# Kernel tuning notes

Measured on AMD Instinct MI355X. Metric: run time of the kernel, lower is better.

The kernel has to match this reference:

```python
import jax, jax.numpy as jnp
import numpy as np

SPATIAL_SHAPES = np.array([[100, 150], [50, 75], [25, 38], [13, 19]], dtype=np.int64)


def setup_inputs() -> dict:
    key = jax.random.key(0)
    k1, k2, k3 = jax.random.split(key, 3)
    B, heads, d = 1, 8, 32
    L, P = SPATIAL_SHAPES.shape[0], 4
    n_tokens = int(SPATIAL_SHAPES.prod(axis=1).sum())  # 19947
    Q = n_tokens
    value = jax.random.normal(k1, (B, n_tokens, heads, d), dtype=jnp.float32)
    sampling_locations = jax.random.uniform(k2, (B, Q, heads, L, P, 2), dtype=jnp.float32)
    aw = jax.random.uniform(k3, (B, Q, heads, L, P), dtype=jnp.float32)
    # normalize like the real module (softmax over L*P); keeps magnitudes realistic
    attention_weights = aw / aw.sum(axis=(-2, -1), keepdims=True)
    level_start = np.concatenate([[0], np.cumsum(SPATIAL_SHAPES.prod(axis=1))[:-1]]).astype(np.int64)
    return {
        'value': value,
        'value_spatial_shapes': jnp.asarray(SPATIAL_SHAPES),
        'value_level_start_index': jnp.asarray(level_start),
        'sampling_locations': sampling_locations,
        'attention_weights': attention_weights,
        'im2col_step': 64,
    }


def _sample_level(v, loc, Hh, Ww):
    """Bilinear grid_sample (align_corners=False, zero padding).
    v:   [B, heads, Hh*Ww, D]
    loc: [B, Q, heads, P, 2] normalized in [0,1]
    returns [B, heads, Q, P, D]
    """
    B, Q, heads, P, _ = loc.shape
    D = v.shape[-1]
    # grid = 2*loc - 1; pixel coord = (grid+1)*size/2 - 0.5  ==  loc*size - 0.5
    x = loc[..., 0] * Ww - 0.5
    y = loc[..., 1] * Hh - 0.5
    x0f = jnp.floor(x)
    y0f = jnp.floor(y)
    wx1 = x - x0f
    wy1 = y - y0f
    x0 = x0f.astype(jnp.int32)
    y0 = y0f.astype(jnp.int32)

    def gather(xi, yi):
        valid = ((xi >= 0) & (xi < Ww) & (yi >= 0) & (yi < Hh)).astype(v.dtype)
        idx = jnp.clip(yi, 0, Hh - 1) * Ww + jnp.clip(xi, 0, Ww - 1)  # [B,Q,heads,P]
        idx_t = idx.transpose(0, 2, 1, 3).reshape(B, heads, Q * P, 1)
        g = jnp.take_along_axis(v, idx_t, axis=2)  # [B,heads,Q*P,D]
        g = g.reshape(B, heads, Q, P, D)
        return g, valid.transpose(0, 2, 1, 3)[..., None]

    g00, m00 = gather(x0, y0)
    g01, m01 = gather(x0 + 1, y0)
    g10, m10 = gather(x0, y0 + 1)
    g11, m11 = gather(x0 + 1, y0 + 1)
    wx1t = wx1.transpose(0, 2, 1, 3)[..., None]
    wy1t = wy1.transpose(0, 2, 1, 3)[..., None]
    wx0t = 1.0 - wx1t
    wy0t = 1.0 - wy1t
    return (g00 * m00 * (wx0t * wy0t) + g01 * m01 * (wx1t * wy0t)
            + g10 * m10 * (wx0t * wy1t) + g11 * m11 * (wx1t * wy1t))


def msda_forward(value, spatial_shapes_np, sampling_locations, attention_weights):
    B, n_tokens, heads, D = value.shape
    Q = sampling_locations.shape[1]
    areas = [int(h) * int(w) for h, w in spatial_shapes_np]
    # value per level as [B, heads, H*W, D]
    v_bhnd = value.transpose(0, 2, 1, 3)  # [B, heads, N, D]
    out = jnp.zeros((B, Q, heads, D), dtype=value.dtype)
    start = 0
    for lvl, (Hh, Ww) in enumerate(spatial_shapes_np):
        Hh, Ww = int(Hh), int(Ww)
        v_l = jax.lax.slice_in_dim(v_bhnd, start, start + Hh * Ww, axis=2)
        loc_l = sampling_locations[:, :, :, lvl]  # [B,Q,heads,P,2]
        sampled = _sample_level(v_l, loc_l, Hh, Ww)  # [B,heads,Q,P,D]
        aw_l = attention_weights[:, :, :, lvl]  # [B,Q,heads,P]
        out = out + jnp.einsum('bhqpd,bqhp->bqhd', sampled, aw_l)
        start += Hh * Ww
    return out.reshape(B, Q, heads * D)


def reference(value, value_spatial_shapes, value_level_start_index, sampling_locations, attention_weights, im2col_step):
    spatial_shapes_np = np.asarray(jax.device_get(value_spatial_shapes))
    return msda_forward(value, spatial_shapes_np, sampling_locations, attention_weights)
```

## Files before the change

### kernel.cpp

```cpp
#include <hip/hip_runtime.h>


typedef float    f32x4 __attribute__((ext_vector_type(4)));
typedef float    f32x8 __attribute__((ext_vector_type(8)));
typedef _Float16 f16x8 __attribute__((ext_vector_type(8)));

constexpr int HEADS = 8;
constexpr int DCH   = 32;
constexpr int NSP   = 16;
constexpr int NQ    = 19947;
constexpr int QPB   = 64;
constexpr int HSTR  = NQ * DCH;
constexpr int NVAL  = NQ * HEADS * DCH;

__global__ __launch_bounds__(256)
void cvt_kernel(const float* __restrict__ value, _Float16* __restrict__ ws)
{
    const int i = blockIdx.x * 256 + threadIdx.x;
    if (i >= NQ * HEADS * 4) return;
    const int c8 = i & 3;
    const int h  = (i >> 2) & 7;
    const int t  = i >> 5;
    const float* src = value + (size_t)t * 256 + h * 32 + c8 * 8;
    const f32x4 a = __builtin_nontemporal_load((const f32x4*)src);
    const f32x4 b = __builtin_nontemporal_load((const f32x4*)(src + 4));
    const f32x8 v = {a.x, a.y, a.z, a.w, b.x, b.y, b.z, b.w};
    const f16x8 o = __builtin_convertvector(v, f16x8);
    *(f16x8*)(ws + (size_t)h * HSTR + t * 32 + c8 * 8) = o;
}

template <bool F16>
__global__ __launch_bounds__(256)
void msda_fwd_kernel(const void* __restrict__ valuev,
                     const float* __restrict__ loc,
                     const float* __restrict__ attw,
                     float* __restrict__ out)
{
    __shared__ float s_loc[QPB][33];
    __shared__ float s_aw [QPB][17];

    const int h    = blockIdx.x & 7;
    const int qblk = blockIdx.x >> 3;
    const int q0   = qblk * QPB;
    const int t    = threadIdx.x;

#pragma unroll
    for (int it = 0; it < 2; ++it) {
        const int idx = t + it * 256;
        const int sub = idx >> 3, j = idx & 7;
        const int q = q0 + sub;
        if (q < NQ) {
            const f32x4 v = __builtin_nontemporal_load(
                (const f32x4*)(loc + ((size_t)(q * HEADS + h)) * (NSP * 2) + j * 4));
            const int l = j >> 1;
            const float fW = (l == 0) ? 150.f : (l == 1) ? 75.f : (l == 2) ? 38.f : 19.f;
            const float fH = (l == 0) ? 100.f : (l == 1) ? 50.f : (l == 2) ? 25.f : 13.f;
            s_loc[sub][j * 4 + 0] = v.x * fW - 0.5f;
            s_loc[sub][j * 4 + 1] = v.y * fH - 0.5f;
            s_loc[sub][j * 4 + 2] = v.z * fW - 0.5f;
            s_loc[sub][j * 4 + 3] = v.w * fH - 0.5f;
        }
    }
    {
        const int sub = t >> 2, j = t & 3;
        const int q = q0 + sub;
        if (q < NQ) {
            const f32x4 w = __builtin_nontemporal_load(
                (const f32x4*)(attw + ((size_t)(q * HEADS + h)) * NSP + j * 4));
            s_aw[sub][j * 4 + 0] = w.x;
            s_aw[sub][j * 4 + 1] = w.y;
            s_aw[sub][j * 4 + 2] = w.z;
            s_aw[sub][j * 4 + 3] = w.w;
        }
    }
    __syncthreads();

    const int sub = t >> 2;
    const int j   = t & 2 * 2;
    const int jj  = t & 3;
    const int q   = q0 + sub;
    if (q >= NQ) return;
    (void)j;

    const _Float16* vf16 = (const _Float16*)valuev + (size_t)h * HSTR + jj * 8;
    const float*    vf32 = (const float*)valuev + h * DCH + jj * 8;

    f32x8 accA = {0.f, 0.f, 0.f, 0.f, 0.f, 0.f, 0.f, 0.f};
    f32x8 accB = {0.f, 0.f, 0.f, 0.f, 0.f, 0.f, 0.f, 0.f};

#pragma unroll
    for (int l = 0; l < 4; ++l) {
        const int W = (l == 0) ? 150 : (l == 1) ? 75 : (l == 2) ? 38 : 19;
        const int H = (l == 0) ? 100 : (l == 1) ? 50 : (l == 2) ? 25 : 13;
        const int S = (l == 0) ? 0 : (l == 1) ? 15000 : (l == 2) ? 18750 : 19700;
#pragma unroll
        for (int p = 0; p < 4; ++p) {
            const int sp = l * 4 + p;
            const float x  = s_loc[sub][sp * 2 + 0];
            const float y  = s_loc[sub][sp * 2 + 1];
            const float aw = s_aw[sub][sp];

            const float x0f = floorf(x);
            const float y0f = floorf(y);
            const float wx1 = x - x0f;
            const float wy1 = y - y0f;
            const float wx0 = 1.f - wx1;
            const float wy0 = 1.f - wy1;

            const int x0 = (int)x0f, y0 = (int)y0f;
            const int x1 = x0 + 1,   y1 = y0 + 1;

            const float awy0 = aw * wy0;
            const float awy1 = aw * wy1;
            const float wx0m = ((unsigned)x0 < (unsigned)W) ? wx0  : 0.f;
            const float wx1m = ((unsigned)x1 < (unsigned)W) ? wx1  : 0.f;
            const float wy0m = ((unsigned)y0 < (unsigned)H) ? awy0 : 0.f;
            const float wy1m = ((unsigned)y1 < (unsigned)H) ? awy1 : 0.f;
            const float c00 = wy0m * wx0m;
            const float c01 = wy0m * wx1m;
            const float c10 = wy1m * wx0m;
            const float c11 = wy1m * wx1m;

            const int cx0 = max(x0, 0), cx1 = min(x1, W - 1);
            const int cy0 = max(y0, 0), cy1 = min(y1, H - 1);
            const int r0 = S + cy0 * W;
            const int r1 = S + cy1 * W;
            const int i00 = r0 + cx0;
            const int i01 = r0 + cx1;
            const int i10 = r1 + cx0;
            const int i11 = r1 + cx1;

            f32x8* accp = (l < 2) ? &accA : &accB;

            if constexpr (F16) {
                const f16x8 g00 = *(const f16x8*)(vf16 + (size_t)i00 * 32);
                const f16x8 g01 = *(const f16x8*)(vf16 + (size_t)i01 * 32);
                const f16x8 g10 = *(const f16x8*)(vf16 + (size_t)i10 * 32);
                const f16x8 g11 = *(const f16x8*)(vf16 + (size_t)i11 * 32);
#pragma unroll
                for (int k = 0; k < 8; ++k) {
                    (*accp)[k] += c00 * (float)g00[k];
                    (*accp)[k] += c01 * (float)g01[k];
                    (*accp)[k] += c10 * (float)g10[k];
                    (*accp)[k] += c11 * (float)g11[k];
                }
            } else {
                const f32x4 a0 = *(const f32x4*)(vf32 + ((size_t)i00 << 8));
                const f32x4 a1 = *(const f32x4*)(vf32 + ((size_t)i00 << 8) + 4);
                const f32x4 b0 = *(const f32x4*)(vf32 + ((size_t)i01 << 8));
                const f32x4 b1 = *(const f32x4*)(vf32 + ((size_t)i01 << 8) + 4);
                const f32x4 c0 = *(const f32x4*)(vf32 + ((size_t)i10 << 8));
                const f32x4 c1 = *(const f32x4*)(vf32 + ((size_t)i10 << 8) + 4);
                const f32x4 d0_ = *(const f32x4*)(vf32 + ((size_t)i11 << 8));
                const f32x4 d1 = *(const f32x4*)(vf32 + ((size_t)i11 << 8) + 4);
#pragma unroll
                for (int k = 0; k < 4; ++k) {
                    (*accp)[k]     += c00 * a0[k] + c01 * b0[k] + c10 * c0[k] + c11 * d0_[k];
                    (*accp)[k + 4] += c00 * a1[k] + c01 * b1[k] + c10 * c1[k] + c11 * d1[k];
                }
            }
        }
    }

    const f32x8 acc = accA + accB;
    float* op = out + (size_t)(q * HEADS + h) * DCH + jj * 8;
    const f32x4 lo = {acc[0], acc[1], acc[2], acc[3]};
    const f32x4 hi = {acc[4], acc[5], acc[6], acc[7]};
    __builtin_nontemporal_store(lo, (f32x4*)op);
    __builtin_nontemporal_store(hi, (f32x4*)(op + 4));
}

extern "C" void kernel_launch(void* const* d_in, const int* in_sizes, int n_in,
                              void* d_out, int out_size, void* d_ws, size_t ws_size,
                              hipStream_t stream) {
    const float* value = (const float*)d_in[0];
    const float* loc   = (const float*)d_in[3];
    const float* attw  = (const float*)d_in[4];
    float* out = (float*)d_out;

    const int qblocks = (NQ + QPB - 1) / QPB;
    const int grid = qblocks * HEADS;

    const size_t f16_bytes = (size_t)NVAL * sizeof(_Float16);
    if (ws_size >= f16_bytes) {
        _Float16* ws = (_Float16*)d_ws;
        const int cgrid = (NQ * HEADS * 4 + 255) / 256;
        cvt_kernel<<<cgrid, 256, 0, stream>>>(value, ws);
        msda_fwd_kernel<true><<<grid, 256, 0, stream>>>(ws, loc, attw, out);
    } else {
        msda_fwd_kernel<false><<<grid, 256, 0, stream>>>(value, loc, attw, out);
    }
}
```

Before: 54.98 us.

## Software-pipeline bilinear gathers and halve block size in MSDA kernel

The sampling loop is flattened over all 16 sampling points. The gathers for point sp+1 are issued before accumulating point sp, so gather latency overlaps FMA work. The forward kernel now uses 128-thread blocks covering 32 queries, doubling the block count for better latency hiding and load balance. The fp16 conversion kernel is remapped so each block handles a single head, making its workspace writes contiguous. The prefetch raises register pressure, and the compiler may already have scheduled the fully unrolled loads this way.

```diff
diff --git a/kernel.cpp b/kernel.cpp
--- a/kernel.cpp
+++ b/kernel.cpp
@@ -9,28 +9,34 @@
 constexpr int DCH   = 32;
 constexpr int NSP   = 16;
 constexpr int NQ    = 19947;
-constexpr int QPB   = 64;
+constexpr int QPB   = 32;
 constexpr int HSTR  = NQ * DCH;
 constexpr int NVAL  = NQ * HEADS * DCH;
+
+__device__ __forceinline__ void lvl_const(int l, int& W, int& H, int& S) {
+    W = (l == 0) ? 150 : (l == 1) ? 75 : (l == 2) ? 38 : 19;
+    H = (l == 0) ? 100 : (l == 1) ? 50 : (l == 2) ? 25 : 13;
+    S = (l == 0) ? 0 : (l == 1) ? 15000 : (l == 2) ? 18750 : 19700;
+}
 
 __global__ __launch_bounds__(256)
 void cvt_kernel(const float* __restrict__ value, _Float16* __restrict__ ws)
 {
-    const int i = blockIdx.x * 256 + threadIdx.x;
-    if (i >= NQ * HEADS * 4) return;
-    const int c8 = i & 3;
-    const int h  = (i >> 2) & 7;
-    const int t  = i >> 5;
-    const float* src = value + (size_t)t * 256 + h * 32 + c8 * 8;
+    const int h = blockIdx.x & 7;
+    const int i = (blockIdx.x >> 3) * 256 + threadIdx.x;
+    if (i >= NQ * 4) return;
+    const int c8  = i & 3;
+    const int tok = i >> 2;
+    const float* src = value + (size_t)tok * 256 + h * 32 + c8 * 8;
     const f32x4 a = __builtin_nontemporal_load((const f32x4*)src);
     const f32x4 b = __builtin_nontemporal_load((const f32x4*)(src + 4));
     const f32x8 v = {a.x, a.y, a.z, a.w, b.x, b.y, b.z, b.w};
-    const f16x8 o = __builtin_convertvector(v, f16x8);
-    *(f16x8*)(ws + (size_t)h * HSTR + t * 32 + c8 * 8) = o;
+    *(f16x8*)(ws + (size_t)h * HSTR + (size_t)tok * 32 + c8 * 8) =
+        __builtin_convertvector(v, f16x8);
 }
 
 template <bool F16>
-__global__ __launch_bounds__(256)
+__global__ __launch_bounds__(128)
 void msda_fwd_kernel(const void* __restrict__ valuev,
                      const float* __restrict__ loc,
                      const float* __restrict__ attw,
@@ -46,7 +52,7 @@
 
 #pragma unroll
     for (int it = 0; it < 2; ++it) {
-        const int idx = t + it * 256;
+        const int idx = t + it * 128;
         const int sub = idx >> 3, j = idx & 7;
         const int q = q0 + sub;
         if (q < NQ) {
@@ -76,93 +82,102 @@
     __syncthreads();
 
     const int sub = t >> 2;
-    const int j   = t & 2 * 2;
     const int jj  = t & 3;
     const int q   = q0 + sub;
     if (q >= NQ) return;
-    (void)j;
 
     const _Float16* vf16 = (const _Float16*)valuev + (size_t)h * HSTR + jj * 8;
     const float*    vf32 = (const float*)valuev + h * DCH + jj * 8;
 
-    f32x8 accA = {0.f, 0.f, 0.f, 0.f, 0.f, 0.f, 0.f, 0.f};
-    f32x8 accB = {0.f, 0.f, 0.f, 0.f, 0.f, 0.f, 0.f, 0.f};
-
-#pragma unroll
-    for (int l = 0; l < 4; ++l) {
-        const int W = (l == 0) ? 150 : (l == 1) ? 75 : (l == 2) ? 38 : 19;
-        const int H = (l == 0) ? 100 : (l == 1) ? 50 : (l == 2) ? 25 : 13;
-        const int S = (l == 0) ? 0 : (l == 1) ? 15000 : (l == 2) ? 18750 : 19700;
-#pragma unroll
-        for (int p = 0; p < 4; ++p) {
-            const int sp = l * 4 + p;
-            const float x  = s_loc[sub][sp * 2 + 0];
-            const float y  = s_loc[sub][sp * 2 + 1];
-            const float aw = s_aw[sub][sp];
-
-            const float x0f = floorf(x);
-            const float y0f = floorf(y);
-            const float wx1 = x - x0f;
-            const float wy1 = y - y0f;
-            const float wx0 = 1.f - wx1;
-            const float wy0 = 1.f - wy1;
-
-            const int x0 = (int)x0f, y0 = (int)y0f;
-            const int x1 = x0 + 1,   y1 = y0 + 1;
-
-            const float awy0 = aw * wy0;
-            const float awy1 = aw * wy1;
-            const float wx0m = ((unsigned)x0 < (unsigned)W) ? wx0  : 0.f;
-            const float wx1m = ((unsigned)x1 < (unsigned)W) ? wx1  : 0.f;
-            const float wy0m = ((unsigned)y0 < (unsigned)H) ? awy0 : 0.f;
-            const float wy1m = ((unsigned)y1 < (unsigned)H) ? awy1 : 0.f;
-            const float c00 = wy0m * wx0m;
-            const float c01 = wy0m * wx1m;
-            const float c10 = wy1m * wx0m;
-            const float c11 = wy1m * wx1m;
-
-            const int cx0 = max(x0, 0), cx1 = min(x1, W - 1);
-            const int cy0 = max(y0, 0), cy1 = min(y1, H - 1);
-            const int r0 = S + cy0 * W;
-            const int r1 = S + cy1 * W;
-            const int i00 = r0 + cx0;
-            const int i01 = r0 + cx1;
-            const int i10 = r1 + cx0;
-            const int i11 = r1 + cx1;
-
-            f32x8* accp = (l < 2) ? &accA : &accB;
-
-            if constexpr (F16) {
-                const f16x8 g00 = *(const f16x8*)(vf16 + (size_t)i00 * 32);
-                const f16x8 g01 = *(const f16x8*)(vf16 + (size_t)i01 * 32);
-                const f16x8 g10 = *(const f16x8*)(vf16 + (size_t)i10 * 32);
-                const f16x8 g11 = *(const f16x8*)(vf16 + (size_t)i11 * 32);
+    auto meta = [&](int sp, f32x4& c, int& i00, int& i01, int& i10, int& i11) {
+        int W, H, S;
+        lvl_const(sp >> 2, W, H, S);
+        const float x  = s_loc[sub][sp * 2 + 0];
+        const float y  = s_loc[sub][sp * 2 + 1];
+        const float aw = s_aw[sub][sp];
+        const float x0f = floorf(x);
+        const float y0f = floorf(y);
+        const float wx1 = x - x0f;
+        const float wy1 = y - y0f;
+        const float wx0 = 1.f - wx1;
+        const float wy0 = 1.f - wy1;
+        const int x0 = (int)x0f, y0 = (int)y0f;
+        const int x1 = x0 + 1,   y1 = y0 + 1;
+        const float wx0m = ((unsigned)x0 < (unsigned)W) ? wx0 : 0.f;
+        const float wx1m = ((unsigned)x1 < (unsigned)W) ? wx1 : 0.f;
+        const float wy0m = ((unsigned)y0 < (unsigned)H) ? aw * wy0 : 0.f;
+        const float wy1m = ((unsigned)y1 < (unsigned)H) ? aw * wy1 : 0.f;
+        c.x = wy0m * wx0m;
+        c.y = wy0m * wx1m;
+        c.z = wy1m * wx0m;
+        c.w = wy1m * wx1m;
+        const int cx0 = max(x0, 0), cx1 = min(x1, W - 1);
+        const int cy0 = max(y0, 0), cy1 = min(y1, H - 1);
+        const int r0 = S + cy0 * W;
+        const int r1 = S + cy1 * W;
+        i00 = r0 + cx0; i01 = r0 + cx1; i10 = r1 + cx0; i11 = r1 + cx1;
+    };
+
+    f32x8 acc = {0.f, 0.f, 0.f, 0.f, 0.f, 0.f, 0.f, 0.f};
+
+    if constexpr (F16) {
+        f32x4 cc;
+        int a00, a01, a10, a11;
+        meta(0, cc, a00, a01, a10, a11);
+        f16x8 g00 = *(const f16x8*)(vf16 + (size_t)a00 * 32);
+        f16x8 g01 = *(const f16x8*)(vf16 + (size_t)a01 * 32);
+        f16x8 g10 = *(const f16x8*)(vf16 + (size_t)a10 * 32);
+        f16x8 g11 = *(const f16x8*)(vf16 + (size_t)a11 * 32);
+#pragma unroll
+        for (int sp = 0; sp < NSP; ++sp) {
+            if (sp + 1 < NSP) {
+                f32x4 cn;
+                int b00, b01, b10, b11;
+                meta(sp + 1, cn, b00, b01, b10, b11);
+                const f16x8 n00 = *(const f16x8*)(vf16 + (size_t)b00 * 32);
+                const f16x8 n01 = *(const f16x8*)(vf16 + (size_t)b01 * 32);
+                const f16x8 n10 = *(const f16x8*)(vf16 + (size_t)b10 * 32);
+                const f16x8 n11 = *(const f16x8*)(vf16 + (size_t)b11 * 32);
 #pragma unroll
                 for (int k = 0; k < 8; ++k) {
-                    (*accp)[k] += c00 * (float)g00[k];
-                    (*accp)[k] += c01 * (float)g01[k];
-                    (*accp)[k] += c10 * (float)g10[k];
-                    (*accp)[k] += c11 * (float)g11[k];
+                    acc[k] += cc.x * (float)g00[k];
+                    acc[k] += cc.y * (float)g01[k];
+                    acc[k] += cc.z * (float)g10[k];
+                    acc[k] += cc.w * (float)g11[k];
                 }
+                cc = cn; g00 = n00; g01 = n01; g10 = n10; g11 = n11;
             } else {
-                const f32x4 a0 = *(const f32x4*)(vf32 + ((size_t)i00 << 8));
-                const f32x4 a1 = *(const f32x4*)(vf32 + ((size_t)i00 << 8) + 4);
-                const f32x4 b0 = *(const f32x4*)(vf32 + ((size_t)i01 << 8));
-                const f32x4 b1 = *(const f32x4*)(vf32 + ((size_t)i01 << 8) + 4);
-                const f32x4 c0 = *(const f32x4*)(vf32 + ((size_t)i10 << 8));
-                const f32x4 c1 = *(const f32x4*)(vf32 + ((size_t)i10 << 8) + 4);
-                const f32x4 d0_ = *(const f32x4*)(vf32 + ((size_t)i11 << 8));
-                const f32x4 d1 = *(const f32x4*)(vf32 + ((size_t)i11 << 8) + 4);
-#pragma unroll
-                for (int k = 0; k < 4; ++k) {
-                    (*accp)[k]     += c00 * a0[k] + c01 * b0[k] + c10 * c0[k] + c11 * d0_[k];
-                    (*accp)[k + 4] += c00 * a1[k] + c01 * b1[k] + c10 * c1[k] + c11 * d1[k];
+#pragma unroll
+                for (int k = 0; k < 8; ++k) {
+                    acc[k] += cc.x * (float)g00[k];
+                    acc[k] += cc.y * (float)g01[k];
+                    acc[k] += cc.z * (float)g10[k];
+                    acc[k] += cc.w * (float)g11[k];
                 }
             }
         }
-    }
-
-    const f32x8 acc = accA + accB;
+    } else {
+#pragma unroll
+        for (int sp = 0; sp < NSP; ++sp) {
+            f32x4 c;
+            int i00, i01, i10, i11;
+            meta(sp, c, i00, i01, i10, i11);
+            const f32x4 a0 = *(const f32x4*)(vf32 + ((size_t)i00 << 8));
+            const f32x4 a1 = *(const f32x4*)(vf32 + ((size_t)i00 << 8) + 4);
+            const f32x4 b0 = *(const f32x4*)(vf32 + ((size_t)i01 << 8));
+            const f32x4 b1 = *(const f32x4*)(vf32 + ((size_t)i01 << 8) + 4);
+            const f32x4 c0 = *(const f32x4*)(vf32 + ((size_t)i10 << 8));
+            const f32x4 c1 = *(const f32x4*)(vf32 + ((size_t)i10 << 8) + 4);
+            const f32x4 d0 = *(const f32x4*)(vf32 + ((size_t)i11 << 8));
+            const f32x4 d1 = *(const f32x4*)(vf32 + ((size_t)i11 << 8) + 4);
+#pragma unroll
+            for (int k = 0; k < 4; ++k) {
+                acc[k]     += c.x * a0[k] + c.y * b0[k] + c.z * c0[k] + c.w * d0[k];
+                acc[k + 4] += c.x * a1[k] + c.y * b1[k] + c.z * c1[k] + c.w * d1[k];
+            }
+        }
+    }
+
     float* op = out + (size_t)(q * HEADS + h) * DCH + jj * 8;
     const f32x4 lo = {acc[0], acc[1], acc[2], acc[3]};
     const f32x4 hi = {acc[4], acc[5], acc[6], acc[7]};
@@ -184,10 +199,10 @@
     const size_t f16_bytes = (size_t)NVAL * sizeof(_Float16);
     if (ws_size >= f16_bytes) {
         _Float16* ws = (_Float16*)d_ws;
-        const int cgrid = (NQ * HEADS * 4 + 255) / 256;
+        const int cgrid = ((NQ * 4 + 255) / 256) * HEADS;
         cvt_kernel<<<cgrid, 256, 0, stream>>>(value, ws);
-        msda_fwd_kernel<true><<<grid, 256, 0, stream>>>(ws, loc, attw, out);
+        msda_fwd_kernel<true><<<grid, 128, 0, stream>>>(ws, loc, attw, out);
     } else {
-        msda_fwd_kernel<false><<<grid, 256, 0, stream>>>(value, loc, attw, out);
-    }
-}
+        msda_fwd_kernel<false><<<grid, 128, 0, stream>>>(value, loc, attw, out);
+    }
+}
```

After: 54.99 us. Within noise of the previous version (+0.0%).
